# Performance work log

Measured on AMD Instinct MI355X. Metric: run time of the kernel, lower is better.

Reference implementation:

```python
import jax, jax.numpy as jnp
import numpy as np

T, N, D, E = 4, 50000, 32, 800000
V_TH = 1.0      # v_threshold
ALPHA = 4.0     # surrogate-gradient sharpness


def setup_inputs() -> dict:
    key = jax.random.key(0)
    k1, k2, k3, k4 = jax.random.split(key, 4)
    s_seq = jax.random.normal(k1, (T, N, D), dtype=jnp.float32) * 0.5
    z_seq = jax.random.normal(k2, (N, D), dtype=jnp.float32) * 0.5
    edge_index = jax.random.randint(k3, (2, E), 0, N, dtype=jnp.int64)
    # GCNConv weight (bias=False), Glorot-ish scale
    W = jax.random.normal(k4, (D, D), dtype=jnp.float32) / np.sqrt(D).astype(np.float32)
    return {"s_seq": s_seq, "z_seq": z_seq, "W": W, "edge_index": edge_index}


def _gcn_conv(x, W, edge_index, n_nodes):
    """PyG GCNConv with add_self_loops=True, normalize=True, bias=False.
    x: [T,N,D]; returns [T,N,D]."""
    src, dst = edge_index[0], edge_index[1]
    ones = jnp.ones(src.shape[0], dtype=x.dtype)
    deg = jax.ops.segment_sum(ones, dst, num_segments=n_nodes) + 1.0  # +1 self loop
    dinv = jax.lax.rsqrt(deg)                                        # [N]
    xw = jnp.einsum('tnd,df->tnf', x, W)                             # dense transform
    norm = dinv[src] * dinv[dst]                                     # [E]
    msgs = xw[:, src, :] * norm[None, :, None]                       # [T,E,D] gather
    agg = jax.vmap(lambda m: jax.ops.segment_sum(m, dst, num_segments=n_nodes))(msgs)
    # self-loop contribution with norm dinv[i]^2
    return agg + xw * (dinv * dinv)[None, :, None]


def _spike(v):
    # Heaviside spike with surrogate (sigmoid) gradient, straight-through.
    s = (v >= V_TH).astype(v.dtype)
    sg = jax.nn.sigmoid(ALPHA * (v - V_TH))
    return s + sg - jax.lax.stop_gradient(sg)


def reference(s_seq, z_seq, W, edge_index):
    n_nodes = s_seq.shape[1]
    x_seq = _gcn_conv(s_seq, W, edge_index, n_nodes)   # [T,N,D]  (dropout p=0.0 is identity)
    y_seq = x_seq.mean(0)                              # temporal mean [N,D]
    # Riemannian IF node: integrate-and-fire over time with soft reset;
    # latent state z drifts by the temporal mean (Euclidean proxy for expmap).
    def step(v, x_t):
        v = v + x_t
        o = _spike(v)
        v = v - o * V_TH
        return v, o
    v0 = jnp.zeros_like(z_seq)
    _, o_seq = jax.lax.scan(step, v0, x_seq)           # [T,N,D]
    z_new = z_seq + y_seq
    return o_seq, z_new
```

## Files before the change

kernel.cpp:

```cpp
#include <hip/hip_runtime.h>
#include <hip/hip_fp16.h>

#define TSTEPS 4
#define DIM 32
#define BINW_SHIFT 8
#define NB 256
#define SP_CH 2048
#define PAD_PER_BIN 772

typedef _Float16 f16x8 __attribute__((ext_vector_type(8)));
typedef float f32x4 __attribute__((ext_vector_type(4)));

__device__ __forceinline__ void ldx8h(const __half* p, float4& lo, float4& hi) {
    uint4 u = *(const uint4*)p;
    __half2 h0 = *(__half2*)&u.x;
    __half2 h1 = *(__half2*)&u.y;
    __half2 h2 = *(__half2*)&u.z;
    __half2 h3 = *(__half2*)&u.w;
    float2 a = __half22float2(h0);
    float2 b = __half22float2(h1);
    float2 c = __half22float2(h2);
    float2 d = __half22float2(h3);
    lo = make_float4(a.x, a.y, b.x, b.y);
    hi = make_float4(c.x, c.y, d.x, d.y);
}

__global__ __launch_bounds__(256) void histgemm_kernel(
    const int* __restrict__ ei, int* __restrict__ ghist,
    const float* __restrict__ s, const float* __restrict__ W,
    __half* __restrict__ xwp, int E, int rows, int N, int nchunks) {
    __shared__ float Wf[32][33];
    int tid = threadIdx.x;

    if ((int)blockIdx.x < nchunks) {
        int* lh = (int*)Wf;
        lh[tid] = 0;
        __syncthreads();
        int beg = blockIdx.x * SP_CH;
        int end = min(beg + SP_CH, E);
        for (int e = beg + tid; e < end; e += 256)
            atomicAdd(&lh[ei[E + e] >> BINW_SHIFT], 1);
        __syncthreads();
        ghist[(size_t)blockIdx.x * NB + tid] = lh[tid];
        return;
    }

    {
        float4 wv = ((const float4*)W)[tid];
        int kk = tid >> 3, c4 = (tid & 7) * 4;
        Wf[kk][c4 + 0] = wv.x; Wf[kk][c4 + 1] = wv.y;
        Wf[kk][c4 + 2] = wv.z; Wf[kk][c4 + 3] = wv.w;
    }
    __syncthreads();

    int lane = tid & 63;
    int wid  = tid >> 6;
    int lrow = lane & 15;
    int kq   = lane >> 4;
    int k0   = kq * 8;

    f16x8 b0, b1;
#pragma unroll
    for (int i = 0; i < 8; i++) {
        b0[i] = (_Float16)Wf[k0 + i][lrow];
        b1[i] = (_Float16)Wf[k0 + i][lrow + 16];
    }

    int rbase = ((int)blockIdx.x - nchunks) * 128 + wid * 32;
#pragma unroll
    for (int rt = 0; rt < 2; rt++) {
        int r = rbase + rt * 16 + lrow;
        f16x8 a;
        if (r < rows) {
            const float4* sp = (const float4*)(s + (size_t)r * 32 + k0);
            float4 u0 = sp[0], u1 = sp[1];
            a[0] = (_Float16)u0.x; a[1] = (_Float16)u0.y;
            a[2] = (_Float16)u0.z; a[3] = (_Float16)u0.w;
            a[4] = (_Float16)u1.x; a[5] = (_Float16)u1.y;
            a[6] = (_Float16)u1.z; a[7] = (_Float16)u1.w;
        } else {
#pragma unroll
            for (int i = 0; i < 8; i++) a[i] = (_Float16)0.f;
        }
        f32x4 c0 = {0.f, 0.f, 0.f, 0.f};
        f32x4 c1 = {0.f, 0.f, 0.f, 0.f};
        c0 = __builtin_amdgcn_mfma_f32_16x16x32_f16(a, b0, c0, 0, 0, 0);
        c1 = __builtin_amdgcn_mfma_f32_16x16x32_f16(a, b1, c1, 0, 0, 0);
        int rr = rbase + rt * 16 + kq * 4;
#pragma unroll
        for (int reg = 0; reg < 4; reg++) {
            int r2 = rr + reg;
            if (r2 < rows) {
                int t = (r2 >= 3 * N) ? 3 : (r2 >= 2 * N) ? 2 : (r2 >= N) ? 1 : 0;
                int n = r2 - t * N;
                __half* dst = xwp + (size_t)n * 128 + t * 32;
                dst[lrow]      = __float2half(c0[reg]);
                dst[lrow + 16] = __float2half(c1[reg]);
            }
        }
    }
}

__global__ __launch_bounds__(512) void colscan_kernel(
    const int* __restrict__ ghist, int* __restrict__ ghist2,
    int* __restrict__ totals, int nchunks) {
    __shared__ int sc[512];
    int t = threadIdx.x;
    int b = blockIdx.x;
    int v = (t < nchunks) ? ghist[(size_t)t * NB + b] : 0;
    sc[t] = v;
    __syncthreads();
    for (int off = 1; off < 512; off <<= 1) {
        int tv = (t >= off) ? sc[t - off] : 0;
        __syncthreads();
        sc[t] += tv;
        __syncthreads();
    }
    if (t < nchunks) ghist2[(size_t)t * NB + b] = sc[t] - v;
    if (t == 511) totals[b] = sc[511];
}

__global__ __launch_bounds__(256) void split_kernel(
    const int* __restrict__ ei, const int* __restrict__ ghist,
    const int* __restrict__ ghist2, const int* __restrict__ totals,
    unsigned int* __restrict__ esorted, int E) {
    __shared__ int binB[NB], pscan[NB], gb[NB], pcur[NB];
    __shared__ unsigned int sbuf[SP_CH];
    int tid = threadIdx.x;
    int bid = blockIdx.x;

    int tot = totals[tid];
    binB[tid] = tot;
    __syncthreads();
    for (int off = 1; off < 256; off <<= 1) {
        int t = (tid >= off) ? binB[tid - off] : 0;
        __syncthreads();
        binB[tid] += t;
        __syncthreads();
    }
    int v = ghist[(size_t)bid * NB + tid];
    pscan[tid] = v;
    __syncthreads();
    for (int off = 1; off < 256; off <<= 1) {
        int t = (tid >= off) ? pscan[tid - off] : 0;
        __syncthreads();
        pscan[tid] += t;
        __syncthreads();
    }
    int pexcl = pscan[tid] - v;
    pscan[tid] = pexcl;
    pcur[tid] = pexcl;
    gb[tid] = (binB[tid] - tot) + ghist2[(size_t)bid * NB + tid] - pexcl;
    __syncthreads();

    int beg = bid * SP_CH;
    int end = min(beg + SP_CH, E);
    int cnt = end - beg;
    for (int e = beg + tid; e < end; e += 256) {
        int sx = ei[e];
        int dx = ei[E + e];
        unsigned int pk = (unsigned int)sx | ((unsigned int)dx << 16);
        int b = dx >> BINW_SHIFT;
        int p = atomicAdd(&pcur[b], 1);
        sbuf[p] = pk;
    }
    __syncthreads();
    for (int idx = tid; idx < cnt; idx += 256) {
        unsigned int e = sbuf[idx];
        int b = e >> 24;
        esorted[gb[b] + idx] = e;
    }
}

__global__ __launch_bounds__(256) void csr_kernel(
    const int* __restrict__ totals, const unsigned int* __restrict__ esorted,
    int* __restrict__ rec, int* __restrict__ offs, int* __restrict__ deg,
    float* __restrict__ dinv, int N) {
    __shared__ int lh[NB], sc[NB], loff[NB], lcur[NB];
    __shared__ int s_ebeg, s_cnt;
    int bin = blockIdx.x;
    int tid = threadIdx.x;
    sc[tid] = totals[tid];
    lh[tid] = 0;
    __syncthreads();
    for (int off = 1; off < 256; off <<= 1) {
        int t = (tid >= off) ? sc[tid - off] : 0;
        __syncthreads();
        sc[tid] += t;
        __syncthreads();
    }
    if (tid == 0) {
        int e0 = bin ? sc[bin - 1] : 0;
        s_ebeg = e0;
        s_cnt = sc[bin] - e0;
    }
    __syncthreads();
    int ebeg = s_ebeg;
    int cnt = s_cnt;
    int gbase = ((ebeg + 3) & ~3) + PAD_PER_BIN * bin;
    for (int i = tid; i < cnt; i += 256)
        atomicAdd(&lh[(esorted[ebeg + i] >> 16) & 255], 1);
    __syncthreads();
    int padded = (lh[tid] + 3) & ~3;
    sc[tid] = padded;
    __syncthreads();
    for (int off = 1; off < 256; off <<= 1) {
        int t = (tid >= off) ? sc[tid - off] : 0;
        __syncthreads();
        sc[tid] += t;
        __syncthreads();
    }
    loff[tid] = sc[tid] - padded;
    lcur[tid] = 0;
    __syncthreads();
    for (int i = tid; i < cnt; i += 256) {
        unsigned int e = esorted[ebeg + i];
        int ln = (e >> 16) & 255;
        int p = atomicAdd(&lcur[ln], 1);
        rec[gbase + loff[ln] + p] = (int)(e & 0xFFFFu);
    }
    int n = (bin << BINW_SHIFT) + tid;
    if (n < N) {
        offs[n] = gbase + loff[tid];
        deg[n] = lh[tid];
        dinv[n] = rsqrtf((float)lh[tid] + 1.0f);
    }
}

__global__ __launch_bounds__(256) void gather_kernel(
    const int* __restrict__ rec, const int* __restrict__ offs,
    const int* __restrict__ deg, const __half* __restrict__ xwp,
    const float* __restrict__ dinv, const float* __restrict__ z,
    float* __restrict__ out, int N) {
    int gid = blockIdx.x * 256 + threadIdx.x;
    int n = gid >> 4;
    if (n >= N) return;
    int wl = threadIdx.x & 63;
    int g = wl >> 4;
    int l = wl & 15;
    long lofs = (long)l * 8;

    float dn = dinv[n];
    int beg = offs[n];
    int cntn = deg[n];

    float4 aLo = make_float4(0.f, 0.f, 0.f, 0.f);
    float4 aHi = make_float4(0.f, 0.f, 0.f, 0.f);
    int i = 0;
    for (; i + 8 <= cntn; i += 8) {
        int4 sa = *(const int4*)(rec + beg + i);
        int4 sb = *(const int4*)(rec + beg + i + 4);
        float n0 = dinv[sa.x] * dn, n1 = dinv[sa.y] * dn;
        float n2 = dinv[sa.z] * dn, n3 = dinv[sa.w] * dn;
        float n4 = dinv[sb.x] * dn, n5 = dinv[sb.y] * dn;
        float n6 = dinv[sb.z] * dn, n7 = dinv[sb.w] * dn;
        float4 l0, h0, l1, h1, l2, h2, l3, h3;
        float4 l4, h4, l5, h5, l6, h6, l7, h7;
        ldx8h(xwp + (long)sa.x * 128 + lofs, l0, h0);
        ldx8h(xwp + (long)sa.y * 128 + lofs, l1, h1);
        ldx8h(xwp + (long)sa.z * 128 + lofs, l2, h2);
        ldx8h(xwp + (long)sa.w * 128 + lofs, l3, h3);
        ldx8h(xwp + (long)sb.x * 128 + lofs, l4, h4);
        ldx8h(xwp + (long)sb.y * 128 + lofs, l5, h5);
        ldx8h(xwp + (long)sb.z * 128 + lofs, l6, h6);
        ldx8h(xwp + (long)sb.w * 128 + lofs, l7, h7);
        aLo.x += n0*l0.x + n1*l1.x + n2*l2.x + n3*l3.x + n4*l4.x + n5*l5.x + n6*l6.x + n7*l7.x;
        aLo.y += n0*l0.y + n1*l1.y + n2*l2.y + n3*l3.y + n4*l4.y + n5*l5.y + n6*l6.y + n7*l7.y;
        aLo.z += n0*l0.z + n1*l1.z + n2*l2.z + n3*l3.z + n4*l4.z + n5*l5.z + n6*l6.z + n7*l7.z;
        aLo.w += n0*l0.w + n1*l1.w + n2*l2.w + n3*l3.w + n4*l4.w + n5*l5.w + n6*l6.w + n7*l7.w;
        aHi.x += n0*h0.x + n1*h1.x + n2*h2.x + n3*h3.x + n4*h4.x + n5*h5.x + n6*h6.x + n7*h7.x;
        aHi.y += n0*h0.y + n1*h1.y + n2*h2.y + n3*h3.y + n4*h4.y + n5*h5.y + n6*h6.y + n7*h7.y;
        aHi.z += n0*h0.z + n1*h1.z + n2*h2.z + n3*h3.z + n4*h4.z + n5*h5.z + n6*h6.z + n7*h7.z;
        aHi.w += n0*h0.w + n1*h1.w + n2*h2.w + n3*h3.w + n4*h4.w + n5*h5.w + n6*h6.w + n7*h7.w;
    }
    for (; i < cntn; i += 4) {
        int4 s4 = *(const int4*)(rec + beg + i);
        int rem = cntn - i;
        int i0 = s4.x;
        int i1 = (rem > 1) ? s4.y : i0;
        int i2 = (rem > 2) ? s4.z : i0;
        int i3 = (rem > 3) ? s4.w : i0;
        float n0 = dinv[i0] * dn;
        float n1 = (rem > 1) ? dinv[i1] * dn : 0.f;
        float n2 = (rem > 2) ? dinv[i2] * dn : 0.f;
        float n3 = (rem > 3) ? dinv[i3] * dn : 0.f;
        float4 l0, h0, l1, h1, l2, h2, l3, h3;
        ldx8h(xwp + (long)i0 * 128 + lofs, l0, h0);
        ldx8h(xwp + (long)i1 * 128 + lofs, l1, h1);
        ldx8h(xwp + (long)i2 * 128 + lofs, l2, h2);
        ldx8h(xwp + (long)i3 * 128 + lofs, l3, h3);
        aLo.x += n0*l0.x + n1*l1.x + n2*l2.x + n3*l3.x;
        aLo.y += n0*l0.y + n1*l1.y + n2*l2.y + n3*l3.y;
        aLo.z += n0*l0.z + n1*l1.z + n2*l2.z + n3*l3.z;
        aLo.w += n0*l0.w + n1*l1.w + n2*l2.w + n3*l3.w;
        aHi.x += n0*h0.x + n1*h1.x + n2*h2.x + n3*h3.x;
        aHi.y += n0*h0.y + n1*h1.y + n2*h2.y + n3*h3.y;
        aHi.z += n0*h0.z + n1*h1.z + n2*h2.z + n3*h3.z;
        aHi.w += n0*h0.w + n1*h1.w + n2*h2.w + n3*h3.w;
    }
    {
        float d2 = dn * dn;
        float4 sl, sh;
        ldx8h(xwp + (long)n * 128 + lofs, sl, sh);
        aLo.x += d2 * sl.x; aLo.y += d2 * sl.y; aLo.z += d2 * sl.z; aLo.w += d2 * sl.w;
        aHi.x += d2 * sh.x; aHi.y += d2 * sh.y; aHi.z += d2 * sh.z; aHi.w += d2 * sh.w;
    }
    float a8[8] = {aLo.x, aLo.y, aLo.z, aLo.w, aHi.x, aHi.y, aHi.z, aHi.w};
    float xs[TSTEPS][8];
    int base = g * 16;
#pragma unroll
    for (int t = 0; t < TSTEPS; t++) {
        int srcLane = base + t * 4 + l;
#pragma unroll
        for (int j = 0; j < 8; j++)
            xs[t][j] = __shfl(a8[j], srcLane, 64);
    }
    if (l < 4) {
        int colBase = n * 32 + l * 8;
        float v[8], y[8];
#pragma unroll
        for (int j = 0; j < 8; j++) {
            v[j] = 0.f;
            y[j] = (xs[0][j] + xs[1][j] + xs[2][j] + xs[3][j]) * 0.25f;
        }
#pragma unroll
        for (int t = 0; t < TSTEPS; t++) {
            float o[8];
#pragma unroll
            for (int j = 0; j < 8; j++) {
                v[j] += xs[t][j];
                o[j] = (v[j] >= 1.0f) ? 1.0f : 0.0f;
                v[j] -= o[j];
            }
            float* dst = out + (size_t)t * N * 32 + colBase;
            *(float4*)dst       = make_float4(o[0], o[1], o[2], o[3]);
            *(float4*)(dst + 4) = make_float4(o[4], o[5], o[6], o[7]);
        }
        float4 zv0 = *(const float4*)(z + colBase);
        float4 zv1 = *(const float4*)(z + colBase + 4);
        float* dst = out + (size_t)TSTEPS * N * 32 + colBase;
        *(float4*)dst       = make_float4(zv0.x + y[0], zv0.y + y[1], zv0.z + y[2], zv0.w + y[3]);
        *(float4*)(dst + 4) = make_float4(zv1.x + y[4], zv1.y + y[5], zv1.z + y[6], zv1.w + y[7]);
    }
}

extern "C" void kernel_launch(void* const* d_in, const int* in_sizes, int n_in,
                              void* d_out, int out_size, void* d_ws, size_t ws_size,
                              hipStream_t stream) {
    const float* s_seq = (const float*)d_in[0];
    const float* z_seq = (const float*)d_in[1];
    const float* W     = (const float*)d_in[2];
    const int*   ei    = (const int*)d_in[3];
    float* out = (float*)d_out;

    int N = in_sizes[1] / DIM;
    int E = in_sizes[3] / 2;
    int rows = TSTEPS * N;
    int nb = (N + 255) >> BINW_SHIFT;
    int nchunks = (E + SP_CH - 1) / SP_CH;

    char* w = (char*)d_ws;
    __half* xwp           = (__half*)w;       w += (size_t)rows * DIM * 2;
    unsigned int* esorted = (unsigned int*)w; w += (size_t)E * 4;
    int*   rec    = (int*)w;  w += ((size_t)E + PAD_PER_BIN * nb + 16) * 4;
    int*   offs   = (int*)w;  w += (size_t)N * 4;
    int*   deg    = (int*)w;  w += (size_t)N * 4;
    float* dinv   = (float*)w; w += (size_t)N * 4;
    int*   ghist  = (int*)w;  w += (size_t)nchunks * NB * 4;
    int*   ghist2 = (int*)w;  w += (size_t)nchunks * NB * 4;
    int*   totals = (int*)w;  w += NB * 4;

    int xwBlocks = (rows + 127) / 128;
    histgemm_kernel<<<nchunks + xwBlocks, 256, 0, stream>>>(
        ei, ghist, s_seq, W, xwp, E, rows, N, nchunks);
    colscan_kernel<<<NB, 512, 0, stream>>>(ghist, ghist2, totals, nchunks);
    split_kernel<<<nchunks, 256, 0, stream>>>(ei, ghist, ghist2, totals, esorted, E);
    csr_kernel<<<nb, 256, 0, stream>>>(totals, esorted, rec, offs, deg, dinv, N);
    gather_kernel<<<(N * 16 + 255) / 256, 256, 0, stream>>>(rec, offs, deg, xwp,
                                                            dinv, z_seq, out, N);
}
```

Before: 155.4 us.

## Prescale XW rows by source dinv to drop per-edge norm loads in gather

Adds a separate degree-count kernel using global atomics so the GEMM stage can multiply each XW row by its source dinv before storing it. The gather kernel then sums neighbor rows without loading dinv per edge and applies the destination dinv once at the end. The GEMM epilogue is also rewritten to swap MFMA operands and store packed half2 vectors instead of scattered scalar halves. The cost is an extra memset, an extra atomic kernel over all edges, and a deg read in the GEMM.

```diff
diff --git a/kernel.cpp b/kernel.cpp
--- a/kernel.cpp
+++ b/kernel.cpp
@@ -25,10 +25,18 @@
     hi = make_float4(c.x, c.y, d.x, d.y);
 }
 
+__global__ __launch_bounds__(256) void deg_kernel(
+    const int* __restrict__ ei, int* __restrict__ deg, int E) {
+    int stride = gridDim.x * 256;
+    for (int e = blockIdx.x * 256 + threadIdx.x; e < E; e += stride)
+        atomicAdd(&deg[ei[E + e]], 1);
+}
+
 __global__ __launch_bounds__(256) void histgemm_kernel(
     const int* __restrict__ ei, int* __restrict__ ghist,
     const float* __restrict__ s, const float* __restrict__ W,
-    __half* __restrict__ xwp, int E, int rows, int N, int nchunks) {
+    const int* __restrict__ deg, __half* __restrict__ xwp,
+    int E, int rows, int N, int nchunks) {
     __shared__ float Wf[32][33];
     int tid = threadIdx.x;
 
@@ -84,19 +92,22 @@
         }
         f32x4 c0 = {0.f, 0.f, 0.f, 0.f};
         f32x4 c1 = {0.f, 0.f, 0.f, 0.f};
-        c0 = __builtin_amdgcn_mfma_f32_16x16x32_f16(a, b0, c0, 0, 0, 0);
-        c1 = __builtin_amdgcn_mfma_f32_16x16x32_f16(a, b1, c1, 0, 0, 0);
-        int rr = rbase + rt * 16 + kq * 4;
-#pragma unroll
-        for (int reg = 0; reg < 4; reg++) {
-            int r2 = rr + reg;
-            if (r2 < rows) {
-                int t = (r2 >= 3 * N) ? 3 : (r2 >= 2 * N) ? 2 : (r2 >= N) ? 1 : 0;
-                int n = r2 - t * N;
-                __half* dst = xwp + (size_t)n * 128 + t * 32;
-                dst[lrow]      = __float2half(c0[reg]);
-                dst[lrow + 16] = __float2half(c1[reg]);
-            }
+        c0 = __builtin_amdgcn_mfma_f32_16x16x32_f16(b0, a, c0, 0, 0, 0);
+        c1 = __builtin_amdgcn_mfma_f32_16x16x32_f16(b1, a, c1, 0, 0, 0);
+        if (r < rows) {
+            int t = (r >= 3 * N) ? 3 : (r >= 2 * N) ? 2 : (r >= N) ? 1 : 0;
+            int n = r - t * N;
+            float di = rsqrtf((float)deg[n] + 1.0f);
+            __half2 p0 = __floats2half2_rn(c0[0] * di, c0[1] * di);
+            __half2 p1 = __floats2half2_rn(c0[2] * di, c0[3] * di);
+            __half2 p2 = __floats2half2_rn(c1[0] * di, c1[1] * di);
+            __half2 p3 = __floats2half2_rn(c1[2] * di, c1[3] * di);
+            __half* dst = xwp + (size_t)n * 128 + t * 32;
+            uint2 u0, u1;
+            u0.x = *(unsigned int*)&p0; u0.y = *(unsigned int*)&p1;
+            u1.x = *(unsigned int*)&p2; u1.y = *(unsigned int*)&p3;
+            *(uint2*)(dst + kq * 4)      = u0;
+            *(uint2*)(dst + 16 + kq * 4) = u1;
         }
     }
 }
@@ -174,7 +185,7 @@
 
 __global__ __launch_bounds__(256) void csr_kernel(
     const int* __restrict__ totals, const unsigned int* __restrict__ esorted,
-    int* __restrict__ rec, int* __restrict__ offs, int* __restrict__ deg,
+    int* __restrict__ rec, int* __restrict__ offs,
     float* __restrict__ dinv, int N) {
     __shared__ int lh[NB], sc[NB], loff[NB], lcur[NB];
     __shared__ int s_ebeg, s_cnt;
@@ -222,7 +233,6 @@
     int n = (bin << BINW_SHIFT) + tid;
     if (n < N) {
         offs[n] = gbase + loff[tid];
-        deg[n] = lh[tid];
         dinv[n] = rsqrtf((float)lh[tid] + 1.0f);
     }
 }
@@ -250,10 +260,6 @@
     for (; i + 8 <= cntn; i += 8) {
         int4 sa = *(const int4*)(rec + beg + i);
         int4 sb = *(const int4*)(rec + beg + i + 4);
-        float n0 = dinv[sa.x] * dn, n1 = dinv[sa.y] * dn;
-        float n2 = dinv[sa.z] * dn, n3 = dinv[sa.w] * dn;
-        float n4 = dinv[sb.x] * dn, n5 = dinv[sb.y] * dn;
-        float n6 = dinv[sb.z] * dn, n7 = dinv[sb.w] * dn;
         float4 l0, h0, l1, h1, l2, h2, l3, h3;
         float4 l4, h4, l5, h5, l6, h6, l7, h7;
         ldx8h(xwp + (long)sa.x * 128 + lofs, l0, h0);
@@ -264,14 +270,14 @@
         ldx8h(xwp + (long)sb.y * 128 + lofs, l5, h5);
         ldx8h(xwp + (long)sb.z * 128 + lofs, l6, h6);
         ldx8h(xwp + (long)sb.w * 128 + lofs, l7, h7);
-        aLo.x += n0*l0.x + n1*l1.x + n2*l2.x + n3*l3.x + n4*l4.x + n5*l5.x + n6*l6.x + n7*l7.x;
-        aLo.y += n0*l0.y + n1*l1.y + n2*l2.y + n3*l3.y + n4*l4.y + n5*l5.y + n6*l6.y + n7*l7.y;
-        aLo.z += n0*l0.z + n1*l1.z + n2*l2.z + n3*l3.z + n4*l4.z + n5*l5.z + n6*l6.z + n7*l7.z;
-        aLo.w += n0*l0.w + n1*l1.w + n2*l2.w + n3*l3.w + n4*l4.w + n5*l5.w + n6*l6.w + n7*l7.w;
-        aHi.x += n0*h0.x + n1*h1.x + n2*h2.x + n3*h3.x + n4*h4.x + n5*h5.x + n6*h6.x + n7*h7.x;
-        aHi.y += n0*h0.y + n1*h1.y + n2*h2.y + n3*h3.y + n4*h4.y + n5*h5.y + n6*h6.y + n7*h7.y;
-        aHi.z += n0*h0.z + n1*h1.z + n2*h2.z + n3*h3.z + n4*h4.z + n5*h5.z + n6*h6.z + n7*h7.z;
-        aHi.w += n0*h0.w + n1*h1.w + n2*h2.w + n3*h3.w + n4*h4.w + n5*h5.w + n6*h6.w + n7*h7.w;
+        aLo.x += (l0.x + l1.x) + (l2.x + l3.x) + (l4.x + l5.x) + (l6.x + l7.x);
+        aLo.y += (l0.y + l1.y) + (l2.y + l3.y) + (l4.y + l5.y) + (l6.y + l7.y);
+        aLo.z += (l0.z + l1.z) + (l2.z + l3.z) + (l4.z + l5.z) + (l6.z + l7.z);
+        aLo.w += (l0.w + l1.w) + (l2.w + l3.w) + (l4.w + l5.w) + (l6.w + l7.w);
+        aHi.x += (h0.x + h1.x) + (h2.x + h3.x) + (h4.x + h5.x) + (h6.x + h7.x);
+        aHi.y += (h0.y + h1.y) + (h2.y + h3.y) + (h4.y + h5.y) + (h6.y + h7.y);
+        aHi.z += (h0.z + h1.z) + (h2.z + h3.z) + (h4.z + h5.z) + (h6.z + h7.z);
+        aHi.w += (h0.w + h1.w) + (h2.w + h3.w) + (h4.w + h5.w) + (h6.w + h7.w);
     }
     for (; i < cntn; i += 4) {
         int4 s4 = *(const int4*)(rec + beg + i);
@@ -280,31 +286,32 @@
         int i1 = (rem > 1) ? s4.y : i0;
         int i2 = (rem > 2) ? s4.z : i0;
         int i3 = (rem > 3) ? s4.w : i0;
-        float n0 = dinv[i0] * dn;
-        float n1 = (rem > 1) ? dinv[i1] * dn : 0.f;
-        float n2 = (rem > 2) ? dinv[i2] * dn : 0.f;
-        float n3 = (rem > 3) ? dinv[i3] * dn : 0.f;
+        float w1 = (rem > 1) ? 1.f : 0.f;
+        float w2 = (rem > 2) ? 1.f : 0.f;
+        float w3 = (rem > 3) ? 1.f : 0.f;
         float4 l0, h0, l1, h1, l2, h2, l3, h3;
         ldx8h(xwp + (long)i0 * 128 + lofs, l0, h0);
         ldx8h(xwp + (long)i1 * 128 + lofs, l1, h1);
         ldx8h(xwp + (long)i2 * 128 + lofs, l2, h2);
         ldx8h(xwp + (long)i3 * 128 + lofs, l3, h3);
-        aLo.x += n0*l0.x + n1*l1.x + n2*l2.x + n3*l3.x;
-        aLo.y += n0*l0.y + n1*l1.y + n2*l2.y + n3*l3.y;
-        aLo.z += n0*l0.z + n1*l1.z + n2*l2.z + n3*l3.z;
-        aLo.w += n0*l0.w + n1*l1.w + n2*l2.w + n3*l3.w;
-        aHi.x += n0*h0.x + n1*h1.x + n2*h2.x + n3*h3.x;
-        aHi.y += n0*h0.y + n1*h1.y + n2*h2.y + n3*h3.y;
-        aHi.z += n0*h0.z + n1*h1.z + n2*h2.z + n3*h3.z;
-        aHi.w += n0*h0.w + n1*h1.w + n2*h2.w + n3*h3.w;
+        aLo.x += l0.x + w1 * l1.x + w2 * l2.x + w3 * l3.x;
+        aLo.y += l0.y + w1 * l1.y + w2 * l2.y + w3 * l3.y;
+        aLo.z += l0.z + w1 * l1.z + w2 * l2.z + w3 * l3.z;
+        aLo.w += l0.w + w1 * l1.w + w2 * l2.w + w3 * l3.w;
+        aHi.x += h0.x + w1 * h1.x + w2 * h2.x + w3 * h3.x;
+        aHi.y += h0.y + w1 * h1.y + w2 * h2.y + w3 * h3.y;
+        aHi.z += h0.z + w1 * h1.z + w2 * h2.z + w3 * h3.z;
+        aHi.w += h0.w + w1 * h1.w + w2 * h2.w + w3 * h3.w;
     }
     {
-        float d2 = dn * dn;
         float4 sl, sh;
         ldx8h(xwp + (long)n * 128 + lofs, sl, sh);
-        aLo.x += d2 * sl.x; aLo.y += d2 * sl.y; aLo.z += d2 * sl.z; aLo.w += d2 * sl.w;
-        aHi.x += d2 * sh.x; aHi.y += d2 * sh.y; aHi.z += d2 * sh.z; aHi.w += d2 * sh.w;
-    }
+        aLo.x += sl.x; aLo.y += sl.y; aLo.z += sl.z; aLo.w += sl.w;
+        aHi.x += sh.x; aHi.y += sh.y; aHi.z += sh.z; aHi.w += sh.w;
+    }
+    aLo.x *= dn; aLo.y *= dn; aLo.z *= dn; aLo.w *= dn;
+    aHi.x *= dn; aHi.y *= dn; aHi.z *= dn; aHi.w *= dn;
+
     float a8[8] = {aLo.x, aLo.y, aLo.z, aLo.w, aHi.x, aHi.y, aHi.z, aHi.w};
     float xs[TSTEPS][8];
     int base = g * 16;
@@ -370,12 +377,15 @@
     int*   ghist2 = (int*)w;  w += (size_t)nchunks * NB * 4;
     int*   totals = (int*)w;  w += NB * 4;
 
+    hipMemsetAsync(deg, 0, (size_t)N * 4, stream);
+
     int xwBlocks = (rows + 127) / 128;
+    deg_kernel<<<512, 256, 0, stream>>>(ei, deg, E);
     histgemm_kernel<<<nchunks + xwBlocks, 256, 0, stream>>>(
-        ei, ghist, s_seq, W, xwp, E, rows, N, nchunks);
+        ei, ghist, s_seq, W, deg, xwp, E, rows, N, nchunks);
     colscan_kernel<<<NB, 512, 0, stream>>>(ghist, ghist2, totals, nchunks);
     split_kernel<<<nchunks, 256, 0, stream>>>(ei, ghist, ghist2, totals, esorted, E);
-    csr_kernel<<<nb, 256, 0, stream>>>(totals, esorted, rec, offs, deg, dinv, N);
+    csr_kernel<<<nb, 256, 0, stream>>>(totals, esorted, rec, offs, dinv, N);
     gather_kernel<<<(N * 16 + 255) / 256, 256, 0, stream>>>(rec, offs, deg, xwp,
                                                             dinv, z_seq, out, N);
 }
```

New measurement: 187.9 us. +20.9%, slower.
